# Performance work log

Hardware: AMD Instinct MI355X
Metric: run time of the kernel (lower is better)

## Reference

```python
import jax, jax.numpy as jnp
import numpy as np

D_MODEL = 1024

def setup_inputs() -> dict:
    key = jax.random.key(0)
    ks = jax.random.split(key, 8)
    B, S, D = 8, 2048, D_MODEL
    scale = 1.0 / np.sqrt(D)
    return {
        "x1": jax.random.normal(ks[0], (B, S, D), dtype=jnp.float32),
        "x2": jax.random.normal(ks[1], (B, S, D), dtype=jnp.float32),
        "Wq": jax.random.normal(ks[2], (D, D), dtype=jnp.float32) * scale,
        "bq": jnp.zeros((D,), dtype=jnp.float32),
        "Wk": jax.random.normal(ks[3], (D, D), dtype=jnp.float32) * scale,
        "bk": jnp.zeros((D,), dtype=jnp.float32),
        "Wv": jax.random.normal(ks[4], (D, D), dtype=jnp.float32) * scale,
        "bv": jnp.zeros((D,), dtype=jnp.float32),
    }

def reference(x1, x2, Wq, bq, Wk, bk, Wv, bv):
    # q1: [B, Sq, D]; k2, v2: [B, Sk, D]
    q1 = jnp.einsum('bsd,de->bse', x1, Wq) + bq
    k2 = jnp.einsum('bsd,de->bse', x2, Wk) + bk
    v2 = jnp.einsum('bsd,de->bse', x2, Wv) + bv
    scale = 1.0 / np.sqrt(q1.shape[-1]).astype(np.float32)
    scores = jnp.einsum('bqd,bkd->bqk', q1, k2) * scale  # [B, Sq, Sk]
    probs = jax.nn.softmax(scores, axis=-1)
    return jnp.einsum('bqk,bkd->bqd', probs, v2)
```

## Files before the change

kernel.cpp:

```cpp
#include <hip/hip_runtime.h>
#include <hip/hip_bf16.h>
#include <hip/hip_fp16.h>

typedef __attribute__((ext_vector_type(8))) short short8;
typedef __attribute__((ext_vector_type(4))) float f32x4;

#define DEVI __device__ __forceinline__

DEVI unsigned short f2bf(float f){
  __hip_bfloat16 h = __float2bfloat16(f);
  unsigned short u; __builtin_memcpy(&u, &h, 2); return u;
}

__global__ void cast_f32_bf16(const float* __restrict__ in, unsigned short* __restrict__ out, int n4){
  int stride = gridDim.x * blockDim.x;
  for (int i = blockIdx.x*blockDim.x + threadIdx.x; i < n4; i += stride){
    float4 f = reinterpret_cast<const float4*>(in)[i];
    ushort4 o;
    o.x = f2bf(f.x); o.y = f2bf(f.y); o.z = f2bf(f.z); o.w = f2bf(f.w);
    reinterpret_cast<ushort4*>(out)[i] = o;
  }
}

__global__ void transpose_cast_w(const float* __restrict__ W, unsigned short* __restrict__ WT, int K, int N){
  __shared__ float tile[32][33];
  int bn = blockIdx.x*32, bk = blockIdx.y*32;
  int tx = threadIdx.x & 31, ty = threadIdx.x >> 5;
  for (int r=0;r<32;r+=8)
    tile[ty+r][tx] = W[(long)(bk+ty+r)*N + bn+tx];
  __syncthreads();
  for (int r=0;r<32;r+=8)
    WT[(long)(bn+ty+r)*K + bk+tx] = (short)f2bf(tile[tx][ty+r]);
}

DEVI void stage16(const short* gsrc, short* lbase, int lane){
#if __has_builtin(__builtin_amdgcn_global_load_lds)
  __builtin_amdgcn_global_load_lds(
      (const __attribute__((address_space(1))) unsigned int*)gsrc,
      (__attribute__((address_space(3))) unsigned int*)lbase, 16, 0, 0);
#else
  reinterpret_cast<short8*>(lbase + lane*8)[0] = *reinterpret_cast<const short8*>(gsrc);
#endif
}

template<int OT, int BIAS>
__global__ __launch_bounds__(256, 2)
void gemm_bt(const short* __restrict__ A, const short* __restrict__ Bt,
             const float* __restrict__ bias, void* __restrict__ Cv,
             int M, int N, int K, long sA, long sB, long sC, float scale)
{
  __shared__ short smem[8192];
  const long bz = blockIdx.z;
  A  += bz * sA;
  Bt += bz * sB;
  const int m0 = blockIdx.x * 128, n0 = blockIdx.y * 128;
  const int t = threadIdx.x, lane = t & 63, w = t >> 6;
  const int wr = w >> 1, wc = w & 1;
  const int la = lane & 15, hk = (lane >> 4) * 8;
  const int aOff = (wr*64 + la)*32 + hk;
  const int bOff = 4096 + (wc*64 + la)*32 + hk;

  const short* srcp[4];
  int loff[4];
  #pragma unroll
  for (int i=0;i<4;i++){
    int ch = w*4 + i;
    int half = ch >> 3, c = ch & 7;
    int row = c*16 + (lane >> 2), col = (lane & 3) * 8;
    srcp[i] = (half ? Bt + (long)(n0 + row)*K : A + (long)(m0 + row)*K) + col;
    loff[i] = ch * 512;
  }

  f32x4 acc[4][4] = {};
  const int nk = K >> 5;
  for (int kt = 0; kt < nk; ++kt){
    #pragma unroll
    for (int i=0;i<4;i++) stage16(srcp[i], &smem[loff[i]], lane);
    __syncthreads();
    short8 a[4], b[4];
    #pragma unroll
    for (int m=0;m<4;m++) a[m] = *reinterpret_cast<const short8*>(&smem[aOff + m*512]);
    #pragma unroll
    for (int n=0;n<4;n++) b[n] = *reinterpret_cast<const short8*>(&smem[bOff + n*512]);
    #pragma unroll
    for (int m=0;m<4;m++)
      #pragma unroll
      for (int n=0;n<4;n++)
        acc[m][n] = __builtin_amdgcn_mfma_f32_16x16x32_bf16(a[m], b[n], acc[m][n], 0, 0, 0);
    __syncthreads();
    #pragma unroll
    for (int i=0;i<4;i++) srcp[i] += 32;
  }

  const int rowb = m0 + wr*64 + (lane>>4)*4;
  const int colb = n0 + wc*64 + la;
  #pragma unroll
  for (int m=0;m<4;m++){
    #pragma unroll
    for (int n=0;n<4;n++){
      const int col = colb + n*16;
      float badd = (BIAS==1) ? bias[col] : 0.0f;
      #pragma unroll
      for (int j=0;j<4;j++){
        const int row = rowb + m*16 + j;
        float v = acc[m][n][j] * scale + badd;
        if (BIAS==2) v += bias[row];
        const long idx = bz*sC + (long)row*N + col;
        if constexpr (OT==0) ((float*)Cv)[idx] = v;
        else if constexpr (OT==1) ((__half*)Cv)[idx] = __float2half(v);
        else ((unsigned short*)Cv)[idx] = f2bf(v);
      }
    }
  }
}

__global__ void softmax_rows(unsigned short* __restrict__ SP, int cols){
  const long row = blockIdx.x;
  unsigned short* rp = SP + row * cols;
  const int t = threadIdx.x, lane = t & 63, w = t >> 6;
  short8 raw = *reinterpret_cast<const short8*>(rp + t*8);
  float v[8];
  #pragma unroll
  for (int i=0;i<8;i++){
    unsigned short us = (unsigned short)raw[i];
    __half h; __builtin_memcpy(&h, &us, 2);
    v[i] = __half2float(h);
  }
  float m = v[0];
  #pragma unroll
  for (int i=1;i<8;i++) m = fmaxf(m, v[i]);
  #pragma unroll
  for (int o=32;o;o>>=1) m = fmaxf(m, __shfl_down(m, o));
  __shared__ float red[8];
  if (lane==0) red[w] = m;
  __syncthreads();
  if (t==0) red[4] = fmaxf(fmaxf(red[0],red[1]), fmaxf(red[2],red[3]));
  __syncthreads();
  const float rowmax = red[4];
  float s = 0.f;
  #pragma unroll
  for (int i=0;i<8;i++){ v[i] = __expf(v[i]-rowmax); s += v[i]; }
  #pragma unroll
  for (int o=32;o;o>>=1) s += __shfl_down(s, o);
  if (lane==0) red[w] = s;
  __syncthreads();
  if (t==0) red[5] = red[0]+red[1]+red[2]+red[3];
  __syncthreads();
  const float inv = 1.0f / red[5];
  short8 outp;
  #pragma unroll
  for (int i=0;i<8;i++) outp[i] = (short)f2bf(v[i]*inv);
  *reinterpret_cast<short8*>(rp + t*8) = outp;
}

extern "C" void kernel_launch(void* const* d_in, const int* in_sizes, int n_in,
                              void* d_out, int out_size, void* d_ws, size_t ws_size,
                              hipStream_t stream)
{
  const int B = 8, S = 2048, D = 1024;
  const int BS = B * S;
  const float* x1 = (const float*)d_in[0];
  const float* x2 = (const float*)d_in[1];
  const float* Wq = (const float*)d_in[2];
  const float* bq = (const float*)d_in[3];
  const float* Wk = (const float*)d_in[4];
  const float* bk = (const float*)d_in[5];
  const float* Wv = (const float*)d_in[6];
  const float* bv = (const float*)d_in[7];

  char* ws = (char*)d_ws;
  const size_t MB = 1024*1024;
  short*          x1b = (short*)(ws);
  short*          x2b = (short*)(ws + 32*MB);
  unsigned short* Sc  = (unsigned short*)ws;
  short*          q   = (short*)(ws + 64*MB);
  short*          k   = (short*)(ws + 96*MB);
  short*          vT  = (short*)(ws + 128*MB);
  short*          WqT = (short*)(ws + 160*MB);
  short*          WkT = (short*)(ws + 162*MB);
  short*          WvT = (short*)(ws + 164*MB);

  cast_f32_bf16<<<4096,256,0,stream>>>(x1, (unsigned short*)x1b, BS*D/4);
  cast_f32_bf16<<<4096,256,0,stream>>>(x2, (unsigned short*)x2b, BS*D/4);
  transpose_cast_w<<<dim3(32,32),256,0,stream>>>(Wq, (unsigned short*)WqT, D, D);
  transpose_cast_w<<<dim3(32,32),256,0,stream>>>(Wk, (unsigned short*)WkT, D, D);
  transpose_cast_w<<<dim3(32,32),256,0,stream>>>(Wv, (unsigned short*)WvT, D, D);

  gemm_bt<2,1><<<dim3(BS/128, D/128, 1),256,0,stream>>>(x2b, WkT, bk, k, BS, D, D, 0,0,0, 1.0f);
  gemm_bt<2,2><<<dim3(D/128, S/128, B),256,0,stream>>>(WvT, x2b, bv, vT, D, S, D,
                                                       0, (long)S*D, (long)D*S, 1.0f);
  gemm_bt<2,1><<<dim3(BS/128, D/128, 1),256,0,stream>>>(x1b, WqT, bq, q, BS, D, D, 0,0,0, 1.0f);
  gemm_bt<1,0><<<dim3(S/128, S/128, B),256,0,stream>>>(q, k, nullptr, Sc, S, S, D,
                                                       (long)S*D, (long)S*D, (long)S*S, 0.03125f);
  softmax_rows<<<BS,256,0,stream>>>(Sc, S);
  gemm_bt<0,0><<<dim3(S/128, D/128, B),256,0,stream>>>((short*)Sc, vT, nullptr, d_out, S, D, S,
                                                       (long)S*S, (long)D*S, (long)S*D, 1.0f);
}
```

Before: 393.0 us.

## Replace GEMM with 256x256 tile, 8-wave, multi-buffered pipelined kernel

Replaces the 128x128 single-buffered GEMM with a 256x256 tile kernel using 512 threads and 128KB of dynamic LDS. The kernel runs a multi-stage global->LDS pipeline with XOR-swizzled layout, interleaved barriers and setprio around the MFMA blocks. Block indices are remapped so that consecutive workgroups are spread across the XCDs. The aim is to raise MFMA utilization and hide memory latency, at the cost of one block per CU because of the large LDS footprint, complex hand-tuned waitcnt logic, and fewer blocks per launch.

```diff
diff --git a/kernel.cpp b/kernel.cpp
--- a/kernel.cpp
+++ b/kernel.cpp
@@ -33,77 +33,126 @@
     WT[(long)(bn+ty+r)*K + bk+tx] = (short)f2bf(tile[tx][ty+r]);
 }
 
-DEVI void stage16(const short* gsrc, short* lbase, int lane){
-#if __has_builtin(__builtin_amdgcn_global_load_lds)
+DEVI void stage16(const short* gsrc, short* lbase){
   __builtin_amdgcn_global_load_lds(
       (const __attribute__((address_space(1))) unsigned int*)gsrc,
       (__attribute__((address_space(3))) unsigned int*)lbase, 16, 0, 0);
-#else
-  reinterpret_cast<short8*>(lbase + lane*8)[0] = *reinterpret_cast<const short8*>(gsrc);
-#endif
+}
+
+DEVI void stage_half(const short* __restrict__ gtile, int ldK, int koff,
+                     short* lds_block, int w, int lane){
+  const int r  = lane >> 2;
+  const int kk = ((lane & 3) * 8) ^ ((lane >= 32) ? 16 : 0);
+  #pragma unroll
+  for (int i = 0; i < 2; ++i){
+    const int c = i*8 + w;
+    const short* src = gtile + (long)(c*16 + r) * ldK + koff + kk;
+    stage16(src, lds_block + c*512);
+  }
+}
+
+DEVI short8 ldsRd(const short* lds, int blk, int rowblk, int lane){
+  const int la = lane & 15;
+  int q = rowblk*1024 + la*64 + ((lane>>4)<<4);
+  q ^= (la >= 8) ? 32 : 0;
+  return *reinterpret_cast<const short8*>(lds + blk*8192 + (q>>1));
 }
 
 template<int OT, int BIAS>
-__global__ __launch_bounds__(256, 2)
-void gemm_bt(const short* __restrict__ A, const short* __restrict__ Bt,
-             const float* __restrict__ bias, void* __restrict__ Cv,
-             int M, int N, int K, long sA, long sB, long sC, float scale)
+__global__ __launch_bounds__(512, 2)
+void gemm8(const short* __restrict__ A, const short* __restrict__ Bt,
+           const float* __restrict__ bias, void* __restrict__ Cv,
+           int N, int K, long sA, long sB, long sC, float scale, int nx, int ny)
 {
-  __shared__ short smem[8192];
-  const long bz = blockIdx.z;
+  extern __shared__ short lds[];
+  const int nwg = gridDim.x;
+  const int cpx = nwg >> 3;
+  const int wg  = (blockIdx.x & 7)*cpx + (blockIdx.x >> 3);
+  const int bx  = wg % nx;
+  const int tmp = wg / nx;
+  const int by  = tmp % ny;
+  const long bz = tmp / ny;
   A  += bz * sA;
   Bt += bz * sB;
-  const int m0 = blockIdx.x * 128, n0 = blockIdx.y * 128;
+  const int m0 = bx * 256, n0 = by * 256;
+  const short* Ab = A  + (long)m0 * K;
+  const short* Bb = Bt + (long)n0 * K;
+
   const int t = threadIdx.x, lane = t & 63, w = t >> 6;
-  const int wr = w >> 1, wc = w & 1;
-  const int la = lane & 15, hk = (lane >> 4) * 8;
-  const int aOff = (wr*64 + la)*32 + hk;
-  const int bOff = 4096 + (wc*64 + la)*32 + hk;
-
-  const short* srcp[4];
-  int loff[4];
-  #pragma unroll
-  for (int i=0;i<4;i++){
-    int ch = w*4 + i;
-    int half = ch >> 3, c = ch & 7;
-    int row = c*16 + (lane >> 2), col = (lane & 3) * 8;
-    srcp[i] = (half ? Bt + (long)(n0 + row)*K : A + (long)(m0 + row)*K) + col;
-    loff[i] = ch * 512;
-  }
-
-  f32x4 acc[4][4] = {};
-  const int nk = K >> 5;
-  for (int kt = 0; kt < nk; ++kt){
+  const int wr = w >> 2, wc = w & 3;
+
+  f32x4 acc[8][4] = {};
+  short8 bv[4];
+
+  const int NT = K >> 6;
+  const int niter = NT >> 1;
+
+  stage_half(Ab, K, 0,  lds + 0,     w, lane);
+  stage_half(Bb, K, 0,  lds + 16384, w, lane);
+  stage_half(Ab, K, 32, lds + 8192,  w, lane);
+  stage_half(Bb, K, 32, lds + 24576, w, lane);
+  stage_half(Ab, K, 64, lds + 32768, w, lane);
+  stage_half(Bb, K, 64, lds + 49152, w, lane);
+  asm volatile("s_waitcnt vmcnt(4)" ::: "memory");
+  __builtin_amdgcn_s_barrier();
+
+#define PH(CBUF, QM, QK, SPTR, SKOFF, SBLK, TAILVM) do {                        \
+    short8 a0_ = ldsRd(lds, (CBUF)*4 + (QK), wr*8 + (QM)*4 + 0, lane);          \
+    short8 a1_ = ldsRd(lds, (CBUF)*4 + (QK), wr*8 + (QM)*4 + 1, lane);          \
+    short8 a2_ = ldsRd(lds, (CBUF)*4 + (QK), wr*8 + (QM)*4 + 2, lane);          \
+    short8 a3_ = ldsRd(lds, (CBUF)*4 + (QK), wr*8 + (QM)*4 + 3, lane);          \
+    if ((QM) == 0){                                                             \
+      bv[0] = ldsRd(lds, (CBUF)*4 + 2 + (QK), wc*4 + 0, lane);                  \
+      bv[1] = ldsRd(lds, (CBUF)*4 + 2 + (QK), wc*4 + 1, lane);                  \
+      bv[2] = ldsRd(lds, (CBUF)*4 + 2 + (QK), wc*4 + 2, lane);                  \
+      bv[3] = ldsRd(lds, (CBUF)*4 + 2 + (QK), wc*4 + 3, lane);                  \
+    }                                                                           \
+    stage_half(SPTR, K, (SKOFF), lds + (SBLK), w, lane);                        \
+    __builtin_amdgcn_s_barrier();                                               \
+    asm volatile("s_waitcnt lgkmcnt(0)" ::: "memory");                          \
+    __builtin_amdgcn_s_setprio(1);                                              \
+    { short8 av_[4] = {a0_, a1_, a2_, a3_};                                     \
+      _Pragma("unroll")                                                         \
+      for (int i_=0;i_<4;i_++){                                                 \
+        _Pragma("unroll")                                                       \
+        for (int j_=0;j_<4;j_++)                                                \
+          acc[(QM)*4+i_][j_] = __builtin_amdgcn_mfma_f32_16x16x32_bf16(         \
+              av_[i_], bv[j_], acc[(QM)*4+i_][j_], 0, 0, 0);                    \
+      }                                                                         \
+    }                                                                           \
+    __builtin_amdgcn_s_setprio(0);                                              \
+    if (TAILVM) asm volatile("s_waitcnt vmcnt(4)" ::: "memory");                \
+    __builtin_amdgcn_s_barrier();                                               \
+  } while(0)
+
+  for (int it = 0; it < niter; ++it){
+    const int u  = it*2;
+    const int k1 = ((u+1) % NT)*64;
+    const int k2 = ((u+2) % NT)*64;
+    const int k3 = ((u+3) % NT)*64;
+    PH(0, 0, 0, Ab, k1+32, 40960, 0);
+    PH(0, 1, 0, Bb, k1+32, 57344, 0);
+    PH(0, 0, 1, Ab, k2,    0,     0);
+    PH(0, 1, 1, Bb, k2,    16384, 1);
+    PH(1, 0, 0, Ab, k2+32, 8192,  0);
+    PH(1, 1, 0, Bb, k2+32, 24576, 0);
+    PH(1, 0, 1, Ab, k3,    32768, 0);
+    PH(1, 1, 1, Bb, k3,    49152, 1);
+  }
+#undef PH
+
+  const int rowb = m0 + wr*128 + ((lane>>4)<<2);
+  const int colb = n0 + wc*64 + (lane & 15);
+  #pragma unroll
+  for (int mi=0; mi<8; ++mi){
     #pragma unroll
-    for (int i=0;i<4;i++) stage16(srcp[i], &smem[loff[i]], lane);
-    __syncthreads();
-    short8 a[4], b[4];
-    #pragma unroll
-    for (int m=0;m<4;m++) a[m] = *reinterpret_cast<const short8*>(&smem[aOff + m*512]);
-    #pragma unroll
-    for (int n=0;n<4;n++) b[n] = *reinterpret_cast<const short8*>(&smem[bOff + n*512]);
-    #pragma unroll
-    for (int m=0;m<4;m++)
-      #pragma unroll
-      for (int n=0;n<4;n++)
-        acc[m][n] = __builtin_amdgcn_mfma_f32_16x16x32_bf16(a[m], b[n], acc[m][n], 0, 0, 0);
-    __syncthreads();
-    #pragma unroll
-    for (int i=0;i<4;i++) srcp[i] += 32;
-  }
-
-  const int rowb = m0 + wr*64 + (lane>>4)*4;
-  const int colb = n0 + wc*64 + la;
-  #pragma unroll
-  for (int m=0;m<4;m++){
-    #pragma unroll
-    for (int n=0;n<4;n++){
-      const int col = colb + n*16;
+    for (int nj=0; nj<4; ++nj){
+      const int col = colb + nj*16;
       float badd = (BIAS==1) ? bias[col] : 0.0f;
       #pragma unroll
       for (int j=0;j<4;j++){
-        const int row = rowb + m*16 + j;
-        float v = acc[m][n][j] * scale + badd;
+        const int row = rowb + mi*16 + j;
+        float v = acc[mi][nj][j] * scale + badd;
         if (BIAS==2) v += bias[row];
         const long idx = bz*sC + (long)row*N + col;
         if constexpr (OT==0) ((float*)Cv)[idx] = v;
@@ -180,19 +229,20 @@
   short*          WkT = (short*)(ws + 162*MB);
   short*          WvT = (short*)(ws + 164*MB);
 
+  const size_t SH = 131072;
+
   cast_f32_bf16<<<4096,256,0,stream>>>(x1, (unsigned short*)x1b, BS*D/4);
   cast_f32_bf16<<<4096,256,0,stream>>>(x2, (unsigned short*)x2b, BS*D/4);
   transpose_cast_w<<<dim3(32,32),256,0,stream>>>(Wq, (unsigned short*)WqT, D, D);
   transpose_cast_w<<<dim3(32,32),256,0,stream>>>(Wk, (unsigned short*)WkT, D, D);
   transpose_cast_w<<<dim3(32,32),256,0,stream>>>(Wv, (unsigned short*)WvT, D, D);
 
-  gemm_bt<2,1><<<dim3(BS/128, D/128, 1),256,0,stream>>>(x2b, WkT, bk, k, BS, D, D, 0,0,0, 1.0f);
-  gemm_bt<2,2><<<dim3(D/128, S/128, B),256,0,stream>>>(WvT, x2b, bv, vT, D, S, D,
-                                                       0, (long)S*D, (long)D*S, 1.0f);
-  gemm_bt<2,1><<<dim3(BS/128, D/128, 1),256,0,stream>>>(x1b, WqT, bq, q, BS, D, D, 0,0,0, 1.0f);
-  gemm_bt<1,0><<<dim3(S/128, S/128, B),256,0,stream>>>(q, k, nullptr, Sc, S, S, D,
-                                                       (long)S*D, (long)S*D, (long)S*S, 0.03125f);
+  gemm8<2,1><<<256, 512, SH, stream>>>(x2b, WkT, bk, k, D, D, 0,0,0, 1.0f, 64, 4);
+  gemm8<2,2><<<256, 512, SH, stream>>>(WvT, x2b, bv, vT, S, D, 0, (long)S*D, (long)D*S, 1.0f, 4, 8);
+  gemm8<2,1><<<256, 512, SH, stream>>>(x1b, WqT, bq, q, D, D, 0,0,0, 1.0f, 64, 4);
+  gemm8<1,0><<<512, 512, SH, stream>>>(q, k, nullptr, Sc, S, D,
+                                       (long)S*D, (long)S*D, (long)S*S, 0.03125f, 8, 8);
   softmax_rows<<<BS,256,0,stream>>>(Sc, S);
-  gemm_bt<0,0><<<dim3(S/128, D/128, B),256,0,stream>>>((short*)Sc, vT, nullptr, d_out, S, D, S,
-                                                       (long)S*S, (long)D*S, (long)S*D, 1.0f);
-}
+  gemm8<0,0><<<256, 512, SH, stream>>>((short*)Sc, vT, nullptr, d_out, D, S,
+                                       (long)S*S, (long)D*S, (long)S*D, 1.0f, 8, 4);
+}
```

Result: faster. 332.0 us (-15.5%).

## Double-buffer GEMM tiles with BK=64, swizzled LDS and XCD-aware block remap

Applied to the files above, without the earlier changes.

Rewrites the shared GEMM body to use a two-stage LDS double buffer holding 64-wide K tiles (64KB dynamic shared memory), so global-to-LDS loads for later tiles overlap MFMA work via explicit vmcnt waits and barriers. Adds an XOR swizzle on LDS offsets to reduce bank conflicts and remaps linear block IDs across the 8 XCDs for better L2 locality. Launch order is also reshuffled so x1/Wq casting happens after the K/V projections. The larger LDS footprint may cut occupancy, and the wraparound prefetch issues redundant loads on the final iterations.

```diff
diff --git a/kernel.cpp b/kernel.cpp
--- a/kernel.cpp
+++ b/kernel.cpp
@@ -33,66 +33,106 @@
     WT[(long)(bn+ty+r)*K + bk+tx] = (short)f2bf(tile[tx][ty+r]);
 }
 
-DEVI void stage16(const short* gsrc, short* lbase, int lane){
-#if __has_builtin(__builtin_amdgcn_global_load_lds)
+DEVI void stage16(const short* gsrc, short* lbase){
   __builtin_amdgcn_global_load_lds(
       (const __attribute__((address_space(1))) unsigned int*)gsrc,
       (__attribute__((address_space(3))) unsigned int*)lbase, 16, 0, 0);
-#else
-  reinterpret_cast<short8*>(lbase + lane*8)[0] = *reinterpret_cast<const short8*>(gsrc);
-#endif
 }
 
 template<int OT, int BIAS>
-__global__ __launch_bounds__(256, 2)
-void gemm_bt(const short* __restrict__ A, const short* __restrict__ Bt,
-             const float* __restrict__ bias, void* __restrict__ Cv,
-             int M, int N, int K, long sA, long sB, long sC, float scale)
+DEVI void gemm_db_body(const short* __restrict__ A, const short* __restrict__ Bt,
+                       const float* __restrict__ bias, void* __restrict__ Cv,
+                       int N, int K, long sA, long sB, long sC, float scale, int nx, int ny)
 {
-  __shared__ short smem[8192];
-  const long bz = blockIdx.z;
-  A  += bz * sA;
-  Bt += bz * sB;
-  const int m0 = blockIdx.x * 128, n0 = blockIdx.y * 128;
+  extern __shared__ short lds[];
+  const int nwg = gridDim.x;
+  const int cpx = nwg >> 3;
+  const int wg  = (blockIdx.x & 7)*cpx + (blockIdx.x >> 3);
+  const int bx  = wg % nx;
+  const int tmp = wg / nx;
+  const int by  = tmp % ny;
+  const long bz = tmp / ny;
+  const int m0 = bx * 128, n0 = by * 128;
+  const short* Ab = A  + bz*sA + (long)m0 * K;
+  const short* Bb = Bt + bz*sB + (long)n0 * K;
+
   const int t = threadIdx.x, lane = t & 63, w = t >> 6;
   const int wr = w >> 1, wc = w & 1;
-  const int la = lane & 15, hk = (lane >> 4) * 8;
-  const int aOff = (wr*64 + la)*32 + hk;
-  const int bOff = 4096 + (wc*64 + la)*32 + hk;
-
-  const short* srcp[4];
-  int loff[4];
-  #pragma unroll
-  for (int i=0;i<4;i++){
-    int ch = w*4 + i;
-    int half = ch >> 3, c = ch & 7;
-    int row = c*16 + (lane >> 2), col = (lane & 3) * 8;
-    srcp[i] = (half ? Bt + (long)(n0 + row)*K : A + (long)(m0 + row)*K) + col;
-    loff[i] = ch * 512;
-  }
+
+  const int rr = lane >> 2;
+  const int kk = ((lane & 3) * 8) ^ ((lane & 32) ? 16 : 0);
+  const long off0 = (long)(( w     )*16 + rr) * K + kk;
+  const long off1 = (long)(( 4 + w )*16 + rr) * K + kk;
+
+  const int la = lane & 15;
+  const int lsw = (la*64 + ((lane>>4)<<4)) ^ ((la>=8)?32:0);
+  const short* AP = lds + (lsw>>1) + wr*2048;
+  const short* BP = lds + (lsw>>1) + 8192 + wc*2048;
 
   f32x4 acc[4][4] = {};
-  const int nk = K >> 5;
-  for (int kt = 0; kt < nk; ++kt){
+  const int NT = K >> 6;
+
+#define STAGEH(BASE, BLK) do {                         \
+    stage16((BASE) + off0, (BLK) + w*512);             \
+    stage16((BASE) + off1, (BLK) + (4+w)*512);         \
+  } while(0)
+#define STAGE(BUF, KB) do {                            \
+    STAGEH(Ab + (KB),      lds + (BUF)*16384 + 0);     \
+    STAGEH(Ab + (KB) + 32, lds + (BUF)*16384 + 4096);  \
+    STAGEH(Bb + (KB),      lds + (BUF)*16384 + 8192);  \
+    STAGEH(Bb + (KB) + 32, lds + (BUF)*16384 + 12288); \
+  } while(0)
+
+  STAGE(0, 0);
+  STAGE(1, 64);
+  asm volatile("s_waitcnt vmcnt(8)" ::: "memory");
+  asm volatile("s_barrier" ::: "memory");
+
+  int cur = 0;
+  for (int u = 0; u < NT; ++u){
+    const short* ap = AP + cur*16384;
+    const short* bp = BP + cur*16384;
     #pragma unroll
-    for (int i=0;i<4;i++) stage16(srcp[i], &smem[loff[i]], lane);
-    __syncthreads();
-    short8 a[4], b[4];
-    #pragma unroll
-    for (int m=0;m<4;m++) a[m] = *reinterpret_cast<const short8*>(&smem[aOff + m*512]);
-    #pragma unroll
-    for (int n=0;n<4;n++) b[n] = *reinterpret_cast<const short8*>(&smem[bOff + n*512]);
-    #pragma unroll
-    for (int m=0;m<4;m++)
-      #pragma unroll
-      for (int n=0;n<4;n++)
-        acc[m][n] = __builtin_amdgcn_mfma_f32_16x16x32_bf16(a[m], b[n], acc[m][n], 0, 0, 0);
-    __syncthreads();
-    #pragma unroll
-    for (int i=0;i<4;i++) srcp[i] += 32;
-  }
-
-  const int rowb = m0 + wr*64 + (lane>>4)*4;
+    for (int kh = 0; kh < 2; ++kh){
+      short8 b0 = *reinterpret_cast<const short8*>(bp + kh*4096 + 0*512);
+      short8 b1 = *reinterpret_cast<const short8*>(bp + kh*4096 + 1*512);
+      short8 b2 = *reinterpret_cast<const short8*>(bp + kh*4096 + 2*512);
+      short8 b3 = *reinterpret_cast<const short8*>(bp + kh*4096 + 3*512);
+      short8 a0 = *reinterpret_cast<const short8*>(ap + kh*4096 + 0*512);
+      short8 a1 = *reinterpret_cast<const short8*>(ap + kh*4096 + 1*512);
+      short8 a2 = *reinterpret_cast<const short8*>(ap + kh*4096 + 2*512);
+      short8 a3 = *reinterpret_cast<const short8*>(ap + kh*4096 + 3*512);
+      acc[0][0] = __builtin_amdgcn_mfma_f32_16x16x32_bf16(a0, b0, acc[0][0],0,0,0);
+      acc[0][1] = __builtin_amdgcn_mfma_f32_16x16x32_bf16(a0, b1, acc[0][1],0,0,0);
+      acc[0][2] = __builtin_amdgcn_mfma_f32_16x16x32_bf16(a0, b2, acc[0][2],0,0,0);
+      acc[0][3] = __builtin_amdgcn_mfma_f32_16x16x32_bf16(a0, b3, acc[0][3],0,0,0);
+      acc[1][0] = __builtin_amdgcn_mfma_f32_16x16x32_bf16(a1, b0, acc[1][0],0,0,0);
+      acc[1][1] = __builtin_amdgcn_mfma_f32_16x16x32_bf16(a1, b1, acc[1][1],0,0,0);
+      acc[1][2] = __builtin_amdgcn_mfma_f32_16x16x32_bf16(a1, b2, acc[1][2],0,0,0);
+      acc[1][3] = __builtin_amdgcn_mfma_f32_16x16x32_bf16(a1, b3, acc[1][3],0,0,0);
+      acc[2][0] = __builtin_amdgcn_mfma_f32_16x16x32_bf16(a2, b0, acc[2][0],0,0,0);
+      acc[2][1] = __builtin_amdgcn_mfma_f32_16x16x32_bf16(a2, b1, acc[2][1],0,0,0);
+      acc[2][2] = __builtin_amdgcn_mfma_f32_16x16x32_bf16(a2, b2, acc[2][2],0,0,0);
+      acc[2][3] = __builtin_amdgcn_mfma_f32_16x16x32_bf16(a2, b3, acc[2][3],0,0,0);
+      acc[3][0] = __builtin_amdgcn_mfma_f32_16x16x32_bf16(a3, b0, acc[3][0],0,0,0);
+      acc[3][1] = __builtin_amdgcn_mfma_f32_16x16x32_bf16(a3, b1, acc[3][1],0,0,0);
+      acc[3][2] = __builtin_amdgcn_mfma_f32_16x16x32_bf16(a3, b2, acc[3][2],0,0,0);
+      acc[3][3] = __builtin_amdgcn_mfma_f32_16x16x32_bf16(a3, b3, acc[3][3],0,0,0);
+    }
+    asm volatile("s_waitcnt lgkmcnt(0)" ::: "memory");
+    asm volatile("s_barrier" ::: "memory");
+    int u2 = u + 2; if (u2 >= NT) u2 -= NT;
+    STAGE(cur, u2*64);
+    asm volatile("s_waitcnt vmcnt(8)" ::: "memory");
+    asm volatile("s_barrier" ::: "memory");
+    cur ^= 1;
+  }
+#undef STAGE
+#undef STAGEH
+
+  asm volatile("s_waitcnt vmcnt(0)" ::: "memory");
+
+  const int rowb = m0 + wr*64 + ((lane>>4)<<2);
   const int colb = n0 + wc*64 + la;
   #pragma unroll
   for (int m=0;m<4;m++){
@@ -114,6 +154,23 @@
   }
 }
 
+#define GATTR __global__ __launch_bounds__(256, 2)
+GATTR void g_proj_k(const short* A, const short* Bt, const float* bias, void* Cv,
+                    int N, int K, long sA, long sB, long sC, float scale, int nx, int ny)
+{ gemm_db_body<2,1>(A,Bt,bias,Cv,N,K,sA,sB,sC,scale,nx,ny); }
+GATTR void g_proj_v(const short* A, const short* Bt, const float* bias, void* Cv,
+                    int N, int K, long sA, long sB, long sC, float scale, int nx, int ny)
+{ gemm_db_body<2,2>(A,Bt,bias,Cv,N,K,sA,sB,sC,scale,nx,ny); }
+GATTR void g_proj_q(const short* A, const short* Bt, const float* bias, void* Cv,
+                    int N, int K, long sA, long sB, long sC, float scale, int nx, int ny)
+{ gemm_db_body<2,1>(A,Bt,bias,Cv,N,K,sA,sB,sC,scale,nx,ny); }
+GATTR void g_score(const short* A, const short* Bt, const float* bias, void* Cv,
+                   int N, int K, long sA, long sB, long sC, float scale, int nx, int ny)
+{ gemm_db_body<1,0>(A,Bt,bias,Cv,N,K,sA,sB,sC,scale,nx,ny); }
+GATTR void g_pv(const short* A, const short* Bt, const float* bias, void* Cv,
+                int N, int K, long sA, long sB, long sC, float scale, int nx, int ny)
+{ gemm_db_body<0,0>(A,Bt,bias,Cv,N,K,sA,sB,sC,scale,nx,ny); }
+
 __global__ void softmax_rows(unsigned short* __restrict__ SP, int cols){
   const long row = blockIdx.x;
   unsigned short* rp = SP + row * cols;
@@ -180,19 +237,19 @@
   short*          WkT = (short*)(ws + 162*MB);
   short*          WvT = (short*)(ws + 164*MB);
 
-  cast_f32_bf16<<<4096,256,0,stream>>>(x1, (unsigned short*)x1b, BS*D/4);
+  const size_t SH = 65536;
+
   cast_f32_bf16<<<4096,256,0,stream>>>(x2, (unsigned short*)x2b, BS*D/4);
-  transpose_cast_w<<<dim3(32,32),256,0,stream>>>(Wq, (unsigned short*)WqT, D, D);
   transpose_cast_w<<<dim3(32,32),256,0,stream>>>(Wk, (unsigned short*)WkT, D, D);
   transpose_cast_w<<<dim3(32,32),256,0,stream>>>(Wv, (unsigned short*)WvT, D, D);
-
-  gemm_bt<2,1><<<dim3(BS/128, D/128, 1),256,0,stream>>>(x2b, WkT, bk, k, BS, D, D, 0,0,0, 1.0f);
-  gemm_bt<2,2><<<dim3(D/128, S/128, B),256,0,stream>>>(WvT, x2b, bv, vT, D, S, D,
-                                                       0, (long)S*D, (long)D*S, 1.0f);
-  gemm_bt<2,1><<<dim3(BS/128, D/128, 1),256,0,stream>>>(x1b, WqT, bq, q, BS, D, D, 0,0,0, 1.0f);
-  gemm_bt<1,0><<<dim3(S/128, S/128, B),256,0,stream>>>(q, k, nullptr, Sc, S, S, D,
-                                                       (long)S*D, (long)S*D, (long)S*S, 0.03125f);
+  g_proj_k<<<1024, 256, SH, stream>>>(x2b, WkT, bk, k, D, D, 0,0,0, 1.0f, 128, 8);
+  g_proj_v<<<1024, 256, SH, stream>>>(WvT, x2b, bv, vT, S, D, 0, (long)S*D, (long)D*S, 1.0f, 8, 16);
+  cast_f32_bf16<<<4096,256,0,stream>>>(x1, (unsigned short*)x1b, BS*D/4);
+  transpose_cast_w<<<dim3(32,32),256,0,stream>>>(Wq, (unsigned short*)WqT, D, D);
+  g_proj_q<<<1024, 256, SH, stream>>>(x1b, WqT, bq, q, D, D, 0,0,0, 1.0f, 128, 8);
+  g_score<<<2048, 256, SH, stream>>>(q, k, nullptr, Sc, S, D,
+                                     (long)S*D, (long)S*D, (long)S*S, 0.03125f, 16, 16);
   softmax_rows<<<BS,256,0,stream>>>(Sc, S);
-  gemm_bt<0,0><<<dim3(S/128, D/128, B),256,0,stream>>>((short*)Sc, vT, nullptr, d_out, S, D, S,
-                                                       (long)S*S, (long)D*S, (long)S*D, 1.0f);
-}
+  g_pv<<<1024, 256, SH, stream>>>((short*)Sc, vT, nullptr, d_out, D, S,
+                                  (long)S*S, (long)D*S, (long)S*D, 1.0f, 16, 8);
+}
```

Measured after the change: 370.5 us. 1.06x faster.
